# Performance work log

Hardware: AMD Instinct MI355X
Metric: run time of the kernel (lower is better)

## Reference

```python
import jax, jax.numpy as jnp
import numpy as np

D = 64
NEG = 0.01            # leakyrelu_neg_slope
X_CONN = 0.25         # x_connection_init
SKIP_H = 0.5          # skip_weight_h
SIGMAS = np.asarray(1.5 ** np.arange(15), np.float32)  # all_sigmas_dist

N_LIG, N_REC = 4096, 8192
E_LIG, E_REC = 65536, 262144
F_LIG, F_REC, NRBF = 15, 27, 15


def _lrelu(x):
    return jax.nn.leaky_relu(x, NEG)


def _ln(x, g, b, eps=1e-5):
    m = x.mean(-1, keepdims=True)
    v = ((x - m) ** 2).mean(-1, keepdims=True)
    return (x - m) * jax.lax.rsqrt(v + eps) * g + b


def _mlp2(x, w1, b1, g, bt, w2, b2):
    # nn.Sequential(Linear, Dropout(0), LeakyReLU, LayerNorm, Linear) in eval mode
    return _ln(_lrelu(x @ w1 + b1), g, bt) @ w2 + b2


def _coords_mlp(m, w1, b1, w2, b2):
    # nn.Sequential(Linear, Dropout(0), LeakyReLU, Linear(out,1))
    return _lrelu(m @ w1 + b1) @ w2 + b2  # [E, 1]


def _seg_mean(v, idx, n):
    # DGL fn.mean over incoming edges at destination nodes (0 for isolated nodes)
    s = jax.ops.segment_sum(v, idx, num_segments=n)
    c = jax.ops.segment_sum(jnp.ones(idx.shape, v.dtype), idx, num_segments=n)
    return s / jnp.maximum(c, 1.0)[:, None]


def setup_inputs() -> dict:
    key = jax.random.key(0)
    ks = iter(jax.random.split(key, 64))

    def n(shape, s=1.0):
        return jax.random.normal(next(ks), shape, jnp.float32) * s

    def lin(i, o):
        return n((i, o), 1.0 / float(np.sqrt(i)))

    zeros = lambda *s: jnp.zeros(s, jnp.float32)
    ones = lambda *s: jnp.ones(s, jnp.float32)

    d = {}
    d['coords_lig'] = n((N_LIG, 3))
    d['h_lig'] = n((N_LIG, D))
    d['orig_h_lig'] = n((N_LIG, D))
    d['orig_coords_lig'] = n((N_LIG, 3))
    d['coords_rec'] = n((N_REC, 3))
    d['h_rec'] = n((N_REC, D))
    d['orig_h_rec'] = n((N_REC, D))
    d['orig_coords_rec'] = n((N_REC, 3))
    d['lig_src'] = jax.random.randint(next(ks), (E_LIG,), 0, N_LIG)
    d['lig_dst'] = jax.random.randint(next(ks), (E_LIG,), 0, N_LIG)
    d['lig_efeat'] = n((E_LIG, F_LIG))
    d['rec_src'] = jax.random.randint(next(ks), (E_REC,), 0, N_REC)
    d['rec_dst'] = jax.random.randint(next(ks), (E_REC,), 0, N_REC)
    d['rec_efeat'] = n((E_REC, F_REC))
    d['mask'] = (jax.random.uniform(next(ks), (N_LIG, N_REC)) < 0.5).astype(jnp.float32)
    # ---- parameters ----
    d['lig_em_w1'], d['lig_em_b1'] = lin(2 * D + F_LIG + NRBF, D), zeros(D)
    d['lig_em_g'], d['lig_em_bt'] = ones(D), zeros(D)
    d['lig_em_w2'], d['lig_em_b2'] = lin(D, D), zeros(D)
    d['rec_em_w1'], d['rec_em_b1'] = lin(2 * D + F_REC + NRBF, D), zeros(D)
    d['rec_em_g'], d['rec_em_bt'] = ones(D), zeros(D)
    d['rec_em_w2'], d['rec_em_b2'] = lin(D, D), zeros(D)
    d['lig_cm_w1'], d['lig_cm_b1'] = lin(D, D), zeros(D)
    d['lig_cm_w2'], d['lig_cm_b2'] = lin(D, 1), zeros(1)
    d['rec_cm_w1'], d['rec_cm_b1'] = lin(D, D), zeros(D)
    d['rec_cm_w2'], d['rec_cm_b2'] = lin(D, 1), zeros(1)
    for nm in ['q_lig_w', 'k_lig_w', 'v_lig_w', 'q_rec_w', 'k_rec_w', 'v_rec_w']:
        d[nm] = lin(D, D)
    d['lig_nm_w1'], d['lig_nm_b1'] = lin(4 * D, D), zeros(D)
    d['lig_nm_g'], d['lig_nm_bt'] = ones(D), zeros(D)
    d['lig_nm_w2'], d['lig_nm_b2'] = lin(D, D), zeros(D)
    d['rec_nm_w1'], d['rec_nm_b1'] = lin(4 * D, D), zeros(D)
    d['rec_nm_g'], d['rec_nm_bt'] = ones(D), zeros(D)
    d['rec_nm_w2'], d['rec_nm_b2'] = lin(D, D), zeros(D)
    return d


def reference(coords_lig, h_lig, orig_h_lig, orig_coords_lig,
              coords_rec, h_rec, orig_h_rec, orig_coords_rec,
              lig_src, lig_dst, lig_efeat, rec_src, rec_dst, rec_efeat, mask,
              lig_em_w1, lig_em_b1, lig_em_g, lig_em_bt, lig_em_w2, lig_em_b2,
              rec_em_w1, rec_em_b1, rec_em_g, rec_em_bt, rec_em_w2, rec_em_b2,
              lig_cm_w1, lig_cm_b1, lig_cm_w2, lig_cm_b2,
              rec_cm_w1, rec_cm_b1, rec_cm_w2, rec_cm_b2,
              q_lig_w, k_lig_w, v_lig_w, q_rec_w, k_rec_w, v_rec_w,
              lig_nm_w1, lig_nm_b1, lig_nm_g, lig_nm_bt, lig_nm_w2, lig_nm_b2,
              rec_nm_w1, rec_nm_b1, rec_nm_g, rec_nm_bt, rec_nm_w2, rec_nm_b2):
    n_lig, n_rec = coords_lig.shape[0], coords_rec.shape[0]
    sig = jnp.asarray(SIGMAS, coords_lig.dtype)

    # --- ligand edge messages: x_rel = x_src - x_dst, multi-scale RBF of |x_rel|^2 ---
    xr_l = coords_lig[lig_src] - coords_lig[lig_dst]                       # [E_l, 3]
    rbf_l = jnp.exp(-jnp.sum(xr_l * xr_l, -1, keepdims=True) / sig)        # [E_l, 15]
    msg_l = _mlp2(jnp.concatenate([h_lig[lig_src], h_lig[lig_dst], lig_efeat, rbf_l], -1),
                  lig_em_w1, lig_em_b1, lig_em_g, lig_em_bt, lig_em_w2, lig_em_b2)

    # --- receptor edge messages (rec_square_distance_scale = 1) ---
    xr_r = coords_rec[rec_src] - coords_rec[rec_dst]
    rbf_r = jnp.exp(-jnp.sum(xr_r * xr_r, -1, keepdims=True) / sig)
    msg_r = _mlp2(jnp.concatenate([h_rec[rec_src], h_rec[rec_dst], rec_efeat, rbf_r], -1),
                  rec_em_w1, rec_em_b1, rec_em_g, rec_em_bt, rec_em_w2, rec_em_b2)

    # --- masked cross-graph attention (pre/post cross-msg norms are identity) ---
    q_l, k_l, v_l = _lrelu(h_lig @ q_lig_w), _lrelu(h_lig @ k_lig_w), h_lig @ v_lig_w
    q_r, k_r, v_r = _lrelu(h_rec @ q_rec_w), _lrelu(h_rec @ k_rec_w), h_rec @ v_rec_w
    s_lr = mask * (q_l @ k_r.T) - 1000.0 * (1.0 - mask)
    att_l = jax.nn.softmax(s_lr, axis=1) @ v_r                             # [N_l, D]
    mt = mask.T
    s_rl = mt * (q_r @ k_l.T) - 1000.0 * (1.0 - mt)
    att_r = jax.nn.softmax(s_rl, axis=1) @ v_l                             # [N_r, D]

    # --- equivariant coordinate update: mean_j phi_x(m_ij) * x_rel, + skip to orig ---
    coef_l = _coords_mlp(msg_l, lig_cm_w1, lig_cm_b1, lig_cm_w2, lig_cm_b2)
    x_lig = X_CONN * orig_coords_lig + (1.0 - X_CONN) * coords_lig + _seg_mean(xr_l * coef_l, lig_dst, n_lig)
    coef_r = _coords_mlp(msg_r, rec_cm_w1, rec_cm_b1, rec_cm_w2, rec_cm_b2)
    x_rec = X_CONN * orig_coords_rec + (1.0 - X_CONN) * coords_rec + _seg_mean(xr_r * coef_r, rec_dst, n_rec)

    # --- node feature update with skip (h_feats_dim == out_feats_dim) ---
    aggr_l = _seg_mean(msg_l, lig_dst, n_lig)
    h_lig_out = SKIP_H * _mlp2(jnp.concatenate([h_lig, aggr_l, att_l, orig_h_lig], -1),
                               lig_nm_w1, lig_nm_b1, lig_nm_g, lig_nm_bt, lig_nm_w2, lig_nm_b2) \
        + (1.0 - SKIP_H) * h_lig
    aggr_r = _seg_mean(msg_r, rec_dst, n_rec)
    h_rec_out = SKIP_H * _mlp2(jnp.concatenate([h_rec, aggr_r, att_r, orig_h_rec], -1),
                               rec_nm_w1, rec_nm_b1, rec_nm_g, rec_nm_bt, rec_nm_w2, rec_nm_b2) \
        + (1.0 - SKIP_H) * h_rec
    return x_lig, h_lig_out, x_rec, h_rec_out
```

## Files before the change

kernel.cpp:

```cpp
#include <hip/hip_runtime.h>
#include <hip/hip_bf16.h>

typedef __hip_bfloat16 bf16;
typedef __attribute__((ext_vector_type(8))) short bfrag8;
typedef __attribute__((ext_vector_type(4))) float f32x4;

#define N_LIG 4096
#define N_REC 8192
#define E_LIG 65536
#define E_REC 262144
#define F_LIGc 15
#define F_RECc 27

__device__ __forceinline__ float ldkv(const float* p, size_t i) { return p[i]; }
__device__ __forceinline__ float ldkv(const bf16* p, size_t i) { return __bfloat162float(p[i]); }
__device__ __forceinline__ short bfbits(float x) {
    bf16 b = __float2bfloat16(x);
    return *(short*)&b;
}
__device__ __forceinline__ unsigned short stg(const float* p, size_t i) {
    return (unsigned short)bfbits(p[i]);
}
__device__ __forceinline__ unsigned short stg(const bf16* p, size_t i) {
    return *(const unsigned short*)(p + i);
// ... 204 lines not shown
        int e = idx / 15, s5 = idx - e * 15;
        xb[e * KP + 128 + F + s5] = bfbits(__expf(-d2s[e] * c_inv_sigma[s5]));
    }
    {
        constexpr int PER = K1S * 32 - IN;
        for (int idx = t; idx < 64 * PER; idx += 256) {
            int e = idx / PER, k = idx - e * PER;
            xb[e * KP + IN + k] = 0;
        }
    }
    __syncthreads();

    float vreg[4][4];
    #pragma unroll
    for (int m = 0; m < 4; ++m) {
        f32x4 acc = {0.f, 0.f, 0.f, 0.f};
        #pragma unroll
        for (int kk = 0; kk < K1S; ++kk) {
            bfrag8 a = *(const bfrag8*)&xb[(m * 16 + lm) * KP + kk * 32 + qd * 8];
            acc = __builtin_amdgcn_mfma_f32_16x16x32_bf16(a, w1f[kk], acc, 0, 0, 0);
        }
        #pragma unroll
        for (int r = 0; r < 4; ++r) {
            float v = acc[r] + b1n;
            v = v > 0.f ? v : 0.01f * v;
            vreg[m][r] = v;
            float a1 = v, a2 = v * v;
            a1 += __shfl_xor(a1, 1); a2 += __shfl_xor(a2, 1);
            a1 += __shfl_xor(a1, 2); a2 += __shfl_xor(a2, 2);
            a1 += __shfl_xor(a1, 4); a2 += __shfl_xor(a2, 4);
            a1 += __shfl_xor(a1, 8); a2 += __shfl_xor(a2, 8);
            if (lm == 0) {
                wsum1[wv][m * 16 + qd * 4 + r] = a1;
                wsum2[wv][m * 16 + qd * 4 + r] = a2;
            }
        }
    }
    __syncthreads();
    if (t < 64) {
        float s1 = wsum1[0][t] + wsum1[1][t] + wsum1[2][t] + wsum1[3][t];
        float s2 = wsum2[0][t] + wsum2[1][t] + wsum2[2][t] + wsum2[3][t];
        float mean = s1 * (1.f / 64.f);
        float var = s2 * (1.f / 64.f) - mean * mean;
        stat_m[t] = mean;
        stat_r[t] = rsqrtf(fmaxf(var, 0.f) + 1e-5f);
    }
    __syncthreads();

    #pragma unroll
    for (int m = 0; m < 4; ++m)
        #pragma unroll
        for (int r = 0; r < 4; ++r) {
            int row = m * 16 + qd * 4 + r;
            float v = (vreg[m][r] - stat_m[row]) * stat_r[row] * gn + btn;
            h1b[row * 72 + n] = bfbits(v);
        }
    __syncthreads();

    f32x4 acc2[4];
    #pragma unroll
    for (int m = 0; m < 4; ++m) {
        f32x4 acc = {0.f, 0.f, 0.f, 0.f};
        #pragma unroll
        for (int kk = 0; kk < 2; ++kk) {
            bfrag8 a = *(const bfrag8*)&h1b[(m * 16 + lm) * 72 + kk * 32 + qd * 8];
            acc = __builtin_amdgcn_mfma_f32_16x16x32_bf16(a, w2f[kk], acc, 0, 0, 0);
        }
        acc2[m] = acc;
    }
    __syncthreads();
    #pragma unroll
    for (int m = 0; m < 4; ++m)
        #pragma unroll
        for (int r = 0; r < 4; ++r)
            msgf[(m * 16 + qd * 4 + r) * 68 + n] = acc2[m][r] + b2n;
    __syncthreads();

    {
        int j = t & 63, q = t >> 6;
        float acc = 0.f;
        #pragma unroll
        for (int e = q * 16; e < q * 16 + 16; ++e) {
            acc += msgf[e * 68 + j];
            bool flush = (e - q * 16 == 15) || (dsts[e + 1] != dsts[e]);
            if (flush) {
                atomicAdd(&aggr[(size_t)dsts[e] * 64 + j], acc);
                acc = 0.f;
            }
        }
    }

    bfrag8 c1f[2];
    #pragma unroll
    for (int kk = 0; kk < 2; ++kk)
        c1f[kk] = *(const bfrag8*)&c1p[((size_t)(kk * 4 + wv) * 64 + L) * 8];
    #pragma unroll
    for (int m = 0; m < 4; ++m) {
        f32x4 acc = {0.f, 0.f, 0.f, 0.f};
        #pragma unroll
        for (int kk = 0; kk < 2; ++kk) {
            const float* mp = &msgf[(m * 16 + lm) * 68 + kk * 32 + qd * 8];
            f32x4 p0 = *(const f32x4*)mp;
            f32x4 p1 = *(const f32x4*)(mp + 4);
            unsigned short tb[8];
            #pragma unroll
            for (int j = 0; j < 4; ++j) {
                tb[j]     = (unsigned short)bfbits(p0[j]);
                tb[4 + j] = (unsigned short)bfbits(p1[j]);
            }
            bfrag8 a = *(bfrag8*)tb;
            acc = __builtin_amdgcn_mfma_f32_16x16x32_bf16(a, c1f[kk], acc, 0, 0, 0);
        }
        #pragma unroll
        for (int r = 0; r < 4; ++r) {
            float v = acc[r] + cb1n;
            v = v > 0.f ? v : 0.01f * v;
            v *= cw2n;
            v += __shfl_xor(v, 1);
            v += __shfl_xor(v, 2);
            v += __shfl_xor(v, 4);
            v += __shfl_xor(v, 8);
            if (lm == 0) coefp[wv][m * 16 + qd * 4 + r] = v;
        }
    }
    __syncthreads();
    if (t < 64)
        coef_all[t] = coefp[0][t] + coefp[1][t] + coefp[2][t] + coefp[3][t] + cb2[0];
    __syncthreads();

    if (t < 12) {
        int q = t / 3, ax = t - q * 3;
        float acc = 0.f;
        for (int e = q * 16; e < q * 16 + 16; ++e) {
            acc += xr_s[e][ax] * coef_all[e];
            bool flush = (e - q * 16 == 15) || (dsts[e + 1] != dsts[e]);
            if (flush) {
                atomicAdd(&xacc[dsts[e] * 3 + ax], acc);
                acc = 0.f;
            }
        }
    }
}

__global__ __launch_bounds__(256, 3) void node_mfma(
    int nbl,
    const float* h1, const float* __restrict__ aggr1, const int* __restrict__ cnt1,
    const float* att1, const float* __restrict__ origh1,
    const float* __restrict__ w1a, const float* __restrict__ b1a,
    const float* __restrict__ ga, const float* __restrict__ bta,
    const float* __restrict__ w2a, const float* __restrict__ b2a, float* out1,
    const float* h2, const float* __restrict__ aggr2, const int* __restrict__ cnt2,
    const float* att2, const float* __restrict__ origh2,
    const float* __restrict__ w1b, const float* __restrict__ b1b,
    const float* __restrict__ gb, const float* __restrict__ btb,
    const float* __restrict__ w2b, const float* __restrict__ b2b, float* out2)
{
    const float *h, *aggr, *att, *orig_h, *w1, *b1, *g, *bt, *w2, *b2;
    const int* cnt;
    float* h_out;
    int n0;
    if ((int)blockIdx.x < nbl) {
        h = h1; aggr = aggr1; cnt = cnt1; att = att1; orig_h = origh1;
        w1 = w1a; b1 = b1a; g = ga; bt = bta; w2 = w2a; b2 = b2a; h_out = out1;
        n0 = blockIdx.x * 64;
    } else {
        h = h2; aggr = aggr2; cnt = cnt2; att = att2; orig_h = origh2;
        w1 = w1b; b1 = b1b; g = gb; bt = btb; w2 = w2b; b2 = b2b; h_out = out2;
        n0 = (blockIdx.x - nbl) * 64;
    }

    constexpr int KP = 264;
    __shared__ __align__(16) char smem[64 * KP * 2];
    __shared__ __align__(16) unsigned short h1b[64 * 72];
    __shared__ float sums[256], sums2[256];
    __shared__ float stat_m[64], stat_r[64];
    unsigned short* xb  = (unsigned short*)smem;
    float*          h1f = (float*)smem;

    const int t  = threadIdx.x;
    const int lm = t & 15;
    const int qd = (t & 63) >> 4;
    const int n  = (t >> 6) * 16 + lm;

    bfrag8 w1f[8], w2f[2];
    #pragma unroll
    for (int kk = 0; kk < 8; ++kk)
        #pragma unroll
        for (int j = 0; j < 8; ++j) {
            int k = kk * 32 + qd * 8 + j;
            w1f[kk][j] = bfbits(w1[k * 64 + n]);
        }
    #pragma unroll
    for (int kk = 0; kk < 2; ++kk)
        #pragma unroll
        for (int j = 0; j < 8; ++j) {
            int k = kk * 32 + qd * 8 + j;
            w2f[kk][j] = bfbits(w2[k * 64 + n]);
        }
    const float b1n = b1[n], b2n = b2[n];

    for (int p = 0; p < 16; ++p) {
        int e = (t >> 6) + 4 * p;
        int node = n0 + e;
        float invc = 1.f / fmaxf((float)cnt[node], 1.f);
        int j = t & 63;
        xb[e * KP + j]       = bfbits(h[(size_t)node * 64 + j]);
        xb[e * KP + 64 + j]  = bfbits(aggr[(size_t)node * 64 + j] * invc);
        xb[e * KP + 128 + j] = bfbits(att[(size_t)node * 64 + j]);
        xb[e * KP + 192 + j] = bfbits(orig_h[(size_t)node * 64 + j]);
    }
    __syncthreads();

    f32x4 acc1[4];
    #pragma unroll
    for (int m = 0; m < 4; ++m) {
        f32x4 acc = {0.f, 0.f, 0.f, 0.f};
        #pragma unroll
        for (int kk = 0; kk < 8; ++kk) {
            bfrag8 a = *(const bfrag8*)&xb[(m * 16 + lm) * KP + kk * 32 + qd * 8];
            acc = __builtin_amdgcn_mfma_f32_16x16x32_bf16(a, w1f[kk], acc, 0, 0, 0);
        }
        acc1[m] = acc;
    }
    __syncthreads();
    #pragma unroll
    for (int m = 0; m < 4; ++m)
        #pragma unroll
        for (int r = 0; r < 4; ++r) {
            int mr = m * 16 + qd * 4 + r;
            float v = acc1[m][r] + b1n;
            v = v > 0.f ? v : 0.01f * v;
            h1f[mr * 68 + n] = v;
        }
    __syncthreads();

    {
        int e = t >> 2, seg = (t & 3) * 16;
        float s1 = 0.f, s2 = 0.f;
        #pragma unroll
        for (int j = 0; j < 16; ++j) {
            float v = h1f[e * 68 + seg + j];
            s1 += v; s2 += v * v;
        }
        sums[t] = s1; sums2[t] = s2;
    }
    __syncthreads();
    if (t < 64) {
        float s1 = sums[4 * t] + sums[4 * t + 1] + sums[4 * t + 2] + sums[4 * t + 3];
        float s2 = sums2[4 * t] + sums2[4 * t + 1] + sums2[4 * t + 2] + sums2[4 * t + 3];
        float mean = s1 * (1.f / 64.f);
        float var = s2 * (1.f / 64.f) - mean * mean;
        stat_m[t] = mean;
        stat_r[t] = rsqrtf(fmaxf(var, 0.f) + 1e-5f);
    }
    __syncthreads();
    for (int idx = t; idx < 4096; idx += 256) {
        int e = idx >> 6, j = idx & 63;
        float v = (h1f[e * 68 + j] - stat_m[e]) * stat_r[e] * g[j] + bt[j];
        h1b[e * 72 + j] = bfbits(v);
    }
    __syncthreads();

    #pragma unroll
    for (int m = 0; m < 4; ++m) {
        f32x4 acc = {0.f, 0.f, 0.f, 0.f};
        #pragma unroll
        for (int kk = 0; kk < 2; ++kk) {
            bfrag8 a = *(const bfrag8*)&h1b[(m * 16 + lm) * 72 + kk * 32 + qd * 8];
            acc = __builtin_amdgcn_mfma_f32_16x16x32_bf16(a, w2f[kk], acc, 0, 0, 0);
        }
        #pragma unroll
        for (int r = 0; r < 4; ++r) {
            int row = n0 + m * 16 + qd * 4 + r;
            float o = acc[r] + b2n;
            float hv = h[(size_t)row * 64 + n];
            h_out[(size_t)row * 64 + n] = 0.5f * o + 0.5f * hv;
        }
    }
}

__global__ __launch_bounds__(256) void kv_proj_kernel(
    const float* __restrict__ h_lig, const float* __restrict__ h_rec,
    const float* __restrict__ kwl, const float* __restrict__ vwl,
    const float* __restrict__ kwr, const float* __restrict__ vwr,
    bf16* __restrict__ kbl, bf16* __restrict__ vbl,
    bf16* __restrict__ kbr, bf16* __restrict__ vbr)
{
    int job = blockIdx.x * 4 + (threadIdx.x >> 6);
    int j = threadIdx.x & 63;
    const float *h, *w; bf16* out; int node, do_l;
    if (job < N_LIG)                { h = h_lig; w = kwl; out = kbl; node = job;                   do_l = 1; }
    else if (job < 2 * N_LIG)       { h = h_lig; w = vwl; out = vbl; node = job - N_LIG;           do_l = 0; }
    else if (job < 2 * N_LIG + N_REC) { h = h_rec; w = kwr; out = kbr; node = job - 2 * N_LIG;     do_l = 1; }
    else                            { h = h_rec; w = vwr; out = vbr; node = job - 2 * N_LIG - N_REC; do_l = 0; }
    float xv = h[(size_t)node * 64 + j];
    float acc = 0.f;
    #pragma unroll
    for (int i = 0; i < 64; ++i) acc += __shfl(xv, i, 64) * w[i * 64 + j];
    if (do_l) acc = acc > 0.f ? acc : 0.01f * acc;
    out[(size_t)node * 64 + j] = __float2bfloat16(acc);
}

__global__ __launch_bounds__(256) void build_masks(
    const float* __restrict__ mask, unsigned char* __restrict__ m8,
    unsigned char* __restrict__ m8T, int R, int C)
{
    __shared__ __align__(16) unsigned char tl[64 * 80];
    int r0 = blockIdx.y * 64, c0 = blockIdx.x * 64;
    int t = threadIdx.x;
    int cs = (t & 15) * 4;
    #pragma unroll
    for (int rr = 0; rr < 4; ++rr) {
        int r = (t >> 4) + rr * 16;
        unsigned b0 = (mask[(size_t)(r0 + r) * C + c0 + cs + 0] != 0.f);
        unsigned b1 = (mask[(size_t)(r0 + r) * C + c0 + cs + 1] != 0.f);
        unsigned b2 = (mask[(size_t)(r0 + r) * C + c0 + cs + 2] != 0.f);
        unsigned b3 = (mask[(size_t)(r0 + r) * C + c0 + cs + 3] != 0.f);
        *(unsigned*)&m8[(size_t)(r0 + r) * C + c0 + cs] = b0 | (b1 << 8) | (b2 << 16) | (b3 << 24);
        tl[(cs + 0) * 80 + r] = (unsigned char)b0;
        tl[(cs + 1) * 80 + r] = (unsigned char)b1;
        tl[(cs + 2) * 80 + r] = (unsigned char)b2;
        tl[(cs + 3) * 80 + r] = (unsigned char)b3;
    }
    __syncthreads();
    {
        int c = t >> 2, rs = (t & 3) * 16;
        *(uint4*)&m8T[(size_t)(c0 + c) * R + r0 + rs] = *(const uint4*)&tl[c * 80 + rs];
    }
}

template <int MMODE>
__global__ __launch_bounds__(256, 4) void attn_mfma(
    int nb1,
    const float* __restrict__ h1, const float* __restrict__ qw1,
    const bf16* __restrict__ k1, const bf16* __restrict__ v1,
    const unsigned char* __restrict__ m81, const float* __restrict__ mf1, long mrs1, long mcs1,
    float* __restrict__ pO1, float* __restrict__ pM1, float* __restrict__ pL1,
    int nrows1, int ncols1, int nsplit1,
    const float* __restrict__ h2, const float* __restrict__ qw2,
    const bf16* __restrict__ k2, const bf16* __restrict__ v2,
    const unsigned char* __restrict__ m82, const float* __restrict__ mf2, long mrs2, long mcs2,
    float* __restrict__ pO2, float* __restrict__ pM2, float* __restrict__ pL2,
    int nrows2, int ncols2, int nsplit2)
{
    const float *h, *qw, *mf;
    const bf16 *kkp, *vvp;
    const unsigned char* m8;
    long mrs, mcs;
    float *pO, *pM, *pL;
    int n_rows, n_cols, nsplit, bid;
    if ((int)blockIdx.x < nb1) {
        h = h1; qw = qw1; kkp = k1; vvp = v1; m8 = m81; mf = mf1; mrs = mrs1; mcs = mcs1;
        pO = pO1; pM = pM1; pL = pL1; n_rows = nrows1; n_cols = ncols1; nsplit = nsplit1;
        bid = blockIdx.x;
    } else {
        h = h2; qw = qw2; kkp = k2; vvp = v2; m8 = m82; mf = mf2; mrs = mrs2; mcs = mcs2;
        pO = pO2; pM = pM2; pL = pL2; n_rows = nrows2; n_cols = ncols2; nsplit = nsplit2;
        bid = blockIdx.x - nb1;
    }

    const int t  = threadIdx.x;
    const int wv = t >> 6;
    const int lm = t & 15;
    const int qd = (t & 63) >> 4;
    const int rb = bid / nsplit;
    const int sp = bid - rb * nsplit;
    const int r0 = rb * 64;
    const int cols_per = n_cols / nsplit;
    const int c_begin = sp * cols_per;

    __shared__ __align__(16) unsigned short sQ[64 * 64];
    __shared__ __align__(16) unsigned short sP[64 * 64];
    __shared__ __align__(16) unsigned short sK[64 * 64];
    __shared__ __align__(16) unsigned short sV[64 * 64];
    __shared__ __align__(16) unsigned char mt[64 * 80];

    const int cP = t >> 3, segP = (t & 7) * 8;
    const int rM = t >> 2, segM = (t & 3) * 16;

    #pragma unroll
    for (int u = 0; u < 2; ++u) {
        int rr = cP + 32 * u;
        const float* hp = h + (size_t)(r0 + rr) * 64 + segP;
        unsigned short tmp[8];
        #pragma unroll
        for (int j = 0; j < 8; ++j) tmp[j] = bfbits(hp[j]);
        *(uint4*)&sP[swz(rr, segP)] = *(uint4*)tmp;
        const float* qp = qw + (size_t)rr * 64 + segP;
        #pragma unroll
        for (int j = 0; j < 8; ++j) sK[swz(segP + j, rr)] = bfbits(qp[j]);
    }

    uint4 kreg[2], vreg[2], mreg;
    kreg[0] = *(const uint4*)(kkp + (size_t)(c_begin + cP) * 64 + segP);
    kreg[1] = *(const uint4*)(kkp + (size_t)(c_begin + cP + 32) * 64 + segP);
    vreg[0] = *(const uint4*)(vvp + (size_t)(c_begin + cP) * 64 + segP);
    vreg[1] = *(const uint4*)(vvp + (size_t)(c_begin + cP + 32) * 64 + segP);
    if (MMODE == 0)
        mreg = *(const uint4*)&m8[(size_t)(r0 + rM) * n_cols + c_begin + segM];
    __syncthreads();

    {
        bfrag8 a0 = *(const bfrag8*)&sP[swz(wv * 16 + lm, qd * 8)];
        bfrag8 a1 = *(const bfrag8*)&sP[swz(wv * 16 + lm, 32 + qd * 8)];
        #pragma unroll
        for (int ns = 0; ns < 4; ++ns) {
            f32x4 acc = {0.f, 0.f, 0.f, 0.f};
            bfrag8 b0 = *(const bfrag8*)&sK[swz(ns * 16 + lm, qd * 8)];
            bfrag8 b1 = *(const bfrag8*)&sK[swz(ns * 16 + lm, 32 + qd * 8)];
            acc = __builtin_amdgcn_mfma_f32_16x16x32_bf16(a0, b0, acc, 0, 0, 0);
            acc = __builtin_amdgcn_mfma_f32_16x16x32_bf16(a1, b1, acc, 0, 0, 0);
            #pragma unroll
            for (int r = 0; r < 4; ++r) {
                float v = acc[r];
                v = v > 0.f ? v : 0.01f * v;
                sQ[swz(wv * 16 + qd * 4 + r, ns * 16 + lm)] = bfbits(v);
            }
        }
    }
    __syncthreads();

    float rm[4], rl[4];
    #pragma unroll
    for (int r = 0; r < 4; ++r) { rm[r] = -1e30f; rl[r] = 0.f; }
    f32x4 o[4];
    #pragma unroll
    for (int ds = 0; ds < 4; ++ds) o[ds] = (f32x4){0.f, 0.f, 0.f, 0.f};

    const int nt = cols_per / 64;
    for (int tile = 0; tile < nt; ++tile) {
        #pragma unroll
        for (int u = 0; u < 2; ++u) {
            *(uint4*)&sK[swz(cP + 32 * u, segP)] = kreg[u];
            unsigned short* pr = (unsigned short*)&vreg[u];
            #pragma unroll
            for (int j = 0; j < 8; ++j) sV[swz(segP + j, cP + 32 * u)] = pr[j];
        }
        if (MMODE == 0) {
            *(uint4*)&mt[rM * 80 + segM] = mreg;
        } else {
            int c0 = c_begin + tile * 64;
            #pragma unroll
            for (int u = 0; u < 16; ++u) {
                int i = t + 256 * u;
                int r = i >> 6, c = i & 63;
                mt[r * 80 + c] = (unsigned char)(
                    mf[(size_t)(r0 + r) * mrs + (size_t)(c0 + c) * mcs] != 0.f);
            }
        }
        __syncthreads();

        if (tile + 1 < nt) {
            int c0n = c_begin + (tile + 1) * 64;
            kreg[0] = *(const uint4*)(kkp + (size_t)(c0n + cP) * 64 + segP);
            kreg[1] = *(const uint4*)(kkp + (size_t)(c0n + cP + 32) * 64 + segP);
            vreg[0] = *(const uint4*)(vvp + (size_t)(c0n + cP) * 64 + segP);
            vreg[1] = *(const uint4*)(vvp + (size_t)(c0n + cP + 32) * 64 + segP);
            if (MMODE == 0)
                mreg = *(const uint4*)&m8[(size_t)(r0 + rM) * n_cols + c0n + segM];
        }

        f32x4 s[4];
        {
            bfrag8 a0 = *(const bfrag8*)&sQ[swz(wv * 16 + lm, qd * 8)];
            bfrag8 a1 = *(const bfrag8*)&sQ[swz(wv * 16 + lm, 32 + qd * 8)];
            #pragma unroll
            for (int ns = 0; ns < 4; ++ns) {
                f32x4 acc = {0.f, 0.f, 0.f, 0.f};
                bfrag8 b0 = *(const bfrag8*)&sK[swz(ns * 16 + lm, qd * 8)];
                bfrag8 b1 = *(const bfrag8*)&sK[swz(ns * 16 + lm, 32 + qd * 8)];
                acc = __builtin_amdgcn_mfma_f32_16x16x32_bf16(a0, b0, acc, 0, 0, 0);
                acc = __builtin_amdgcn_mfma_f32_16x16x32_bf16(a1, b1, acc, 0, 0, 0);
                s[ns] = acc;
            }
        }

        float alpha[4];
        #pragma unroll
        for (int r = 0; r < 4; ++r) {
            int rloc = wv * 16 + qd * 4 + r;
            float v0 = mt[rloc * 80 +  0 + lm] ? s[0][r] : -1000.f;
            float v1 = mt[rloc * 80 + 16 + lm] ? s[1][r] : -1000.f;
            float v2 = mt[rloc * 80 + 32 + lm] ? s[2][r] : -1000.f;
            float v3 = mt[rloc * 80 + 48 + lm] ? s[3][r] : -1000.f;
            float mx = quad_max(fmaxf(fmaxf(v0, v1), fmaxf(v2, v3)));
            float mn = fmaxf(rm[r], mx);
            float al = __expf(rm[r] - mn);
            rm[r] = mn; alpha[r] = al;
            float p0 = __expf(v0 - mn), p1 = __expf(v1 - mn);
            float p2 = __expf(v2 - mn), p3 = __expf(v3 - mn);
            sP[swz(rloc,  0 + lm)] = bfbits(p0);
            sP[swz(rloc, 16 + lm)] = bfbits(p1);
            sP[swz(rloc, 32 + lm)] = bfbits(p2);
            sP[swz(rloc, 48 + lm)] = bfbits(p3);
            float ls = quad_sum(p0 + p1 + p2 + p3);
            rl[r] = rl[r] * al + ls;
        }
        #pragma unroll
        for (int ds = 0; ds < 4; ++ds)
            #pragma unroll
            for (int r = 0; r < 4; ++r) o[ds][r] *= alpha[r];

        __builtin_amdgcn_wave_barrier();
        asm volatile("" ::: "memory");

        {
            bfrag8 a0 = *(const bfrag8*)&sP[swz(wv * 16 + lm, qd * 8)];
            bfrag8 a1 = *(const bfrag8*)&sP[swz(wv * 16 + lm, 32 + qd * 8)];
            #pragma unroll
            for (int ds = 0; ds < 4; ++ds) {
                bfrag8 b0 = *(const bfrag8*)&sV[swz(ds * 16 + lm, qd * 8)];
                bfrag8 b1 = *(const bfrag8*)&sV[swz(ds * 16 + lm, 32 + qd * 8)];
                o[ds] = __builtin_amdgcn_mfma_f32_16x16x32_bf16(a0, b0, o[ds], 0, 0, 0);
                o[ds] = __builtin_amdgcn_mfma_f32_16x16x32_bf16(a1, b1, o[ds], 0, 0, 0);
            }
        }
        __syncthreads();
    }

    #pragma unroll
    for (int ds = 0; ds < 4; ++ds)
        #pragma unroll
        for (int r = 0; r < 4; ++r) {
            int row = r0 + wv * 16 + qd * 4 + r;
            pO[((size_t)sp * n_rows + row) * 64 + ds * 16 + lm] = o[ds][r];
        }
    if (lm == 0) {
        #pragma unroll
        for (int r = 0; r < 4; ++r) {
            int row = r0 + wv * 16 + qd * 4 + r;
            pM[(size_t)sp * n_rows + row] = rm[r];
            pL[(size_t)sp * n_rows + row] = rl[r];
        }
    }
}

__global__ __launch_bounds__(64) void attn_merge2(
    const float* __restrict__ pO1, const float* __restrict__ pM1, const float* __restrict__ pL1,
    float* __restrict__ out1, int ns1,
    const float* __restrict__ pO2, const float* __restrict__ pM2, const float* __restrict__ pL2,
    float* __restrict__ out2, int ns2)
{
    int r = blockIdx.x;
    const float *pO, *pM, *pL; float* out; int n_rows, nsplit;
    if (r < N_LIG) { pO = pO1; pM = pM1; pL = pL1; out = out1; n_rows = N_LIG; nsplit = ns1; }
    else { r -= N_LIG; pO = pO2; pM = pM2; pL = pL2; out = out2; n_rows = N_REC; nsplit = ns2; }
    int d = threadIdx.x;
    float mstar = -1e30f;
    for (int s = 0; s < nsplit; ++s) mstar = fmaxf(mstar, pM[(size_t)s * n_rows + r]);
    float L = 0.f, O = 0.f;
    for (int s = 0; s < nsplit; ++s) {
        float w = __expf(pM[(size_t)s * n_rows + r] - mstar);
        L += pL[(size_t)s * n_rows + r] * w;
        O += pO[((size_t)s * n_rows + r) * 64 + d] * w;
    }
    out[(size_t)r * 64 + d] = O / L;
}

__global__ __launch_bounds__(256) void attn_row_kernel(
    const float* __restrict__ h, const float* __restrict__ qw,
    const bf16* __restrict__ k, const bf16* __restrict__ v,
    const float* __restrict__ mask, long mrs, long mcs,
    float* __restrict__ out, int n_cols)
{
    int row = blockIdx.x;
    int tid = threadIdx.x;
    extern __shared__ float sc[];
    __shared__ float hrow[64];
    __shared__ float qrow[64];
    __shared__ float red[4];
    __shared__ float opart[4][64];

    if (tid < 64) hrow[tid] = h[(size_t)row * 64 + tid];
    __syncthreads();
    if (tid < 64) {
        float a = 0.f;
        #pragma unroll 8
        for (int i = 0; i < 64; ++i) a += hrow[i] * qw[i * 64 + tid];
        qrow[tid] = a > 0.f ? a : 0.01f * a;
    }
    __syncthreads();

    float lmax = -1e30f;
    for (int c = tid; c < n_cols; c += 256) {
        const bf16* kr = k + (size_t)c * 64;
        float s = 0.f;
        #pragma unroll 8
        for (int i = 0; i < 64; ++i) s += qrow[i] * ldkv(kr, i);
        float m = mask[(size_t)row * mrs + (size_t)c * mcs];
        s = m * s - 1000.f * (1.f - m);
        sc[c] = s;
        lmax = fmaxf(lmax, s);
    }
    #pragma unroll
    for (int o = 32; o > 0; o >>= 1) lmax = fmaxf(lmax, __shfl_xor(lmax, o, 64));
    int wid = tid >> 6;
    if ((tid & 63) == 0) red[wid] = lmax;
    __syncthreads();
    float bmax = fmaxf(fmaxf(red[0], red[1]), fmaxf(red[2], red[3]));
    __syncthreads();

    float lsum = 0.f;
    for (int c = tid; c < n_cols; c += 256) {
        float e = __expf(sc[c] - bmax);
        sc[c] = e;
        lsum += e;
    }
    lsum = wave_sum(lsum);
    if ((tid & 63) == 0) red[wid] = lsum;
    __syncthreads();
    float inv = 1.f / (red[0] + red[1] + red[2] + red[3]);

    int dd = tid & 63;
    float o = 0.f;
    for (int c = wid; c < n_cols; c += 4) o += sc[c] * ldkv(v, (size_t)c * 64 + dd);
    opart[wid][dd] = o;
    __syncthreads();
    if (wid == 0)
        out[(size_t)row * 64 + dd] =
            (opart[0][dd] + opart[1][dd] + opart[2][dd] + opart[3][dd]) * inv;
}

__global__ void coord2_kernel(
    const float* __restrict__ ol, const float* __restrict__ cl,
    const float* __restrict__ xl, const int* __restrict__ cntl, float* __restrict__ outl,
    const float* __restrict__ orr, const float* __restrict__ cr,
    const float* __restrict__ xr, const int* __restrict__ cntr, float* __restrict__ outr)
{
    int i = blockIdx.x * 256 + threadIdx.x;
    if (i < N_LIG * 3) {
        int node = i / 3;
        float invc = 1.f / fmaxf((float)cntl[node], 1.f);
        outl[i] = 0.25f * ol[i] + 0.75f * cl[i] + xl[i] * invc;
        return;
    }
    i -= N_LIG * 3;
    if (i < N_REC * 3) {
        int node = i / 3;
        float invc = 1.f / fmaxf((float)cntr[node], 1.f);
        outr[i] = 0.25f * orr[i] + 0.75f * cr[i] + xr[i] * invc;
    }
}

extern "C" void kernel_launch(void* const* d_in, const int* in_sizes, int n_in,
                              void* d_out, int out_size, void* d_ws, size_t ws_size,
                              hipStream_t stream)
{
    const float* coords_lig      = (const float*)d_in[0];
    const float* h_lig           = (const float*)d_in[1];
    const float* orig_h_lig      = (const float*)d_in[2];
    const float* orig_coords_lig = (const float*)d_in[3];
    const float* coords_rec      = (const float*)d_in[4];
    const float* h_rec           = (const float*)d_in[5];
    const float* orig_h_rec      = (const float*)d_in[6];
    const float* orig_coords_rec = (const float*)d_in[7];
    const int* lig_src   = (const int*)d_in[8];
    const int* lig_dst   = (const int*)d_in[9];
    const float* lig_efeat = (const float*)d_in[10];
    const int* rec_src   = (const int*)d_in[11];
    const int* rec_dst   = (const int*)d_in[12];
    const float* rec_efeat = (const float*)d_in[13];
    const float* mask      = (const float*)d_in[14];
    const float *lig_em_w1 = (const float*)d_in[15], *lig_em_b1 = (const float*)d_in[16];
    const float *lig_em_g  = (const float*)d_in[17], *lig_em_bt = (const float*)d_in[18];
    const float *lig_em_w2 = (const float*)d_in[19], *lig_em_b2 = (const float*)d_in[20];
    const float *rec_em_w1 = (const float*)d_in[21], *rec_em_b1 = (const float*)d_in[22];
    const float *rec_em_g  = (const float*)d_in[23], *rec_em_bt = (const float*)d_in[24];
    const float *rec_em_w2 = (const float*)d_in[25], *rec_em_b2 = (const float*)d_in[26];
    const float *lig_cm_w1 = (const float*)d_in[27], *lig_cm_b1 = (const float*)d_in[28];
    const float *lig_cm_w2 = (const float*)d_in[29], *lig_cm_b2 = (const float*)d_in[30];
    const float *rec_cm_w1 = (const float*)d_in[31], *rec_cm_b1 = (const float*)d_in[32];
    const float *rec_cm_w2 = (const float*)d_in[33], *rec_cm_b2 = (const float*)d_in[34];
    const float *q_lig_w = (const float*)d_in[35], *k_lig_w = (const float*)d_in[36];
    const float *v_lig_w = (const float*)d_in[37], *q_rec_w = (const float*)d_in[38];
    const float *k_rec_w = (const float*)d_in[39], *v_rec_w = (const float*)d_in[40];
    const float *lig_nm_w1 = (const float*)d_in[41], *lig_nm_b1 = (const float*)d_in[42];
    const float *lig_nm_g  = (const float*)d_in[43], *lig_nm_bt = (const float*)d_in[44];
    const float *lig_nm_w2 = (const float*)d_in[45], *lig_nm_b2 = (const float*)d_in[46];
    const float *rec_nm_w1 = (const float*)d_in[47], *rec_nm_b1 = (const float*)d_in[48];
    const float *rec_nm_g  = (const float*)d_in[49], *rec_nm_bt = (const float*)d_in[50];
    const float *rec_nm_w2 = (const float*)d_in[51], *rec_nm_b2 = (const float*)d_in[52];

    char* wsb = (char*)d_ws;
    float* aggr_l = (float*)(wsb + 16);
    float* aggr_r = aggr_l + (size_t)N_LIG * 64;
    float* xacc_l = aggr_r + (size_t)N_REC * 64;
    float* xacc_r = xacc_l + (size_t)N_LIG * 3;
    int* counts_l = (int*)(xacc_r + (size_t)N_REC * 3);
    int* counts_r = counts_l + N_LIG;
    const size_t zero_floats =
        (size_t)N_LIG * 64 + (size_t)N_REC * 64 + N_LIG * 3 + N_REC * 3 + N_LIG + N_REC;
    int* cursor_l = counts_r + N_REC;
    int* cursor_r = cursor_l + N_LIG;
    int* order_l  = cursor_r + N_REC;
    int* order_r  = order_l + E_LIG;
    unsigned short* p_rec1  = (unsigned short*)(order_r + E_REC);
    unsigned short* p_lig1  = p_rec1 + 6 * 2048;
    unsigned short* p_rec2  = p_lig1 + 5 * 2048;
    unsigned short* p_lig2  = p_rec2 + 2 * 2048;
    unsigned short* pc_rec1 = p_lig2 + 2 * 2048;
    unsigned short* pc_lig1 = pc_rec1 + 2 * 2048;
    char* kv_base = (char*)(pc_lig1 + 2 * 2048);
    const size_t core_b = (size_t)(kv_base - wsb);
    const size_t kv_b = (size_t)(N_LIG + N_REC) * 64 * 2 * 2;
    const size_t m8_b = (size_t)N_LIG * N_REC;

    const size_t part_b_hi = ((size_t)8 * N_LIG * 64 + (size_t)4 * N_REC * 64) * 4
                           + ((size_t)8 * N_LIG + (size_t)4 * N_REC) * 2 * 4;
    const size_t part_b_lo = ((size_t)4 * N_LIG * 64 + (size_t)2 * N_REC * 64) * 4
                           + ((size_t)4 * N_LIG + (size_t)2 * N_REC) * 2 * 4;

    int tier, ns1, ns2;
    size_t part_b;
    if (ws_size >= core_b + kv_b + part_b_hi + 2 * m8_b) {
        tier = 0; ns1 = 8; ns2 = 4; part_b = part_b_hi;
    } else if (ws_size >= core_b + kv_b + part_b_lo + 2 * m8_b) {
        tier = 0; ns1 = 4; ns2 = 2; part_b = part_b_lo;
    } else if (ws_size >= core_b + kv_b + part_b_lo) {
        tier = 1; ns1 = 4; ns2 = 2; part_b = part_b_lo;
    } else {
        tier = 2; ns1 = 4; ns2 = 2; part_b = part_b_lo;
    }

    bf16* kb_l = (bf16*)kv_base;
    bf16* vb_l = kb_l + (size_t)N_LIG * 64;
    bf16* kb_r = vb_l + (size_t)N_LIG * 64;
    bf16* vb_r = kb_r + (size_t)N_REC * 64;
    float* pO1 = (float*)(kv_base + kv_b);
    float* pO2 = pO1 + (size_t)ns1 * N_LIG * 64;
    float* pM1 = pO2 + (size_t)ns2 * N_REC * 64;
    float* pL1 = pM1 + (size_t)ns1 * N_LIG;
    float* pM2 = pL1 + (size_t)ns1 * N_LIG;
    float* pL2 = pM2 + (size_t)ns2 * N_REC;
    unsigned char* m8  = (unsigned char*)(kv_base + kv_b + part_b);
    unsigned char* m8T = m8 + m8_b;
    bf16* hb_l  = (bf16*)m8;
    bf16* hb_r  = hb_l + (size_t)N_LIG * 64;
    bf16* efb_l = hb_r + (size_t)N_REC * 64;
    bf16* efb_r = efb_l + (size_t)E_LIG * F_LIGc;

    float* out = (float*)d_out;
    float* x_lig_o = out;
    float* h_lig_o = out + 12288;
    float* x_rec_o = out + 274432;
    float* h_rec_o = out + 299008;

    zero_kernel<<<((int)zero_floats + 255) / 256, 256, 0, stream>>>(aggr_l, (int)zero_floats);

    pack_frags<<<19, 256, 0, stream>>>(
        rec_em_w1, lig_em_w1, rec_em_w2, lig_em_w2, rec_cm_w1, lig_cm_w1,
        p_rec1, p_lig1, p_rec2, p_lig2, pc_rec1, pc_lig1);

    hist2_kernel<<<(E_LIG + E_REC) / 256, 256, 0, stream>>>(lig_dst, rec_dst, counts_l, counts_r);
    scan2_kernel<<<2, 256, 0, stream>>>(counts_l, cursor_l, counts_r, cursor_r);
    scatter2_kernel<<<(E_LIG + E_REC) / 256, 256, 0, stream>>>(
        lig_dst, rec_dst, cursor_l, cursor_r, order_l, order_r);

    kv_proj_kernel<<<(2 * (N_LIG + N_REC)) / 4, 256, 0, stream>>>(
        h_lig, h_rec, k_lig_w, v_lig_w, k_rec_w, v_rec_w,
        kb_l, vb_l, kb_r, vb_r);

    if (tier == 0) {
        cvt4_kernel<<<(N_LIG * 64 + N_REC * 64 + E_LIG * F_LIGc + E_REC * F_RECc + 255) / 256,
                      256, 0, stream>>>(
            h_lig, hb_l, N_LIG * 64, h_rec, hb_r, N_REC * 64,
            lig_efeat, efb_l, E_LIG * F_LIGc, rec_efeat, efb_r, E_REC * F_RECc);
        edge_mfma<F_LIGc, 5, bf16><<<E_LIG / 64, 256, 0, stream>>>(
            order_l, coords_lig, hb_l, lig_src, lig_dst, efb_l,
            p_lig1, lig_em_b1, lig_em_g, lig_em_bt, p_lig2, lig_em_b2,
            pc_lig1, lig_cm_b1, lig_cm_w2, lig_cm_b2,
            aggr_l, xacc_l);
        edge_mfma<F_RECc, 6, bf16><<<E_REC / 64, 256, 0, stream>>>(
            order_r, coords_rec, hb_r, rec_src, rec_dst, efb_r,
            p_rec1, rec_em_b1, rec_em_g, rec_em_bt, p_rec2, rec_em_b2,
            pc_rec1, rec_cm_b1, rec_cm_w2, rec_cm_b2,
            aggr_r, xacc_r);
    } else {
        edge_mfma<F_LIGc, 5, float><<<E_LIG / 64, 256, 0, stream>>>(
            order_l, coords_lig, h_lig, lig_src, lig_dst, lig_efeat,
            p_lig1, lig_em_b1, lig_em_g, lig_em_bt, p_lig2, lig_em_b2,
            pc_lig1, lig_cm_b1, lig_cm_w2, lig_cm_b2,
            aggr_l, xacc_l);
        edge_mfma<F_RECc, 6, float><<<E_REC / 64, 256, 0, stream>>>(
            order_r, coords_rec, h_rec, rec_src, rec_dst, rec_efeat,
            p_rec1, rec_em_b1, rec_em_g, rec_em_bt, p_rec2, rec_em_b2,
            pc_rec1, rec_cm_b1, rec_cm_w2, rec_cm_b2,
            aggr_r, xacc_r);
    }

    const int nb1 = (N_LIG / 64) * ns1;
    const int nb2 = (N_REC / 64) * ns2;
    if (tier <= 1) {
        if (tier == 0) {
            dim3 bg(N_REC / 64, N_LIG / 64);
            build_masks<<<bg, 256, 0, stream>>>(mask, m8, m8T, N_LIG, N_REC);
            attn_mfma<0><<<nb1 + nb2, 256, 0, stream>>>(
                nb1,
                h_lig, q_lig_w, kb_r, vb_r, m8, mask, 0L, 0L,
                pO1, pM1, pL1, N_LIG, N_REC, ns1,
                h_rec, q_rec_w, kb_l, vb_l, m8T, mask, 0L, 0L,
                pO2, pM2, pL2, N_REC, N_LIG, ns2);
        } else {
            attn_mfma<1><<<nb1 + nb2, 256, 0, stream>>>(
                nb1,
                h_lig, q_lig_w, kb_r, vb_r, (const unsigned char*)0, mask, (long)N_REC, 1L,
                pO1, pM1, pL1, N_LIG, N_REC, ns1,
                h_rec, q_rec_w, kb_l, vb_l, (const unsigned char*)0, mask, 1L, (long)N_REC,
                pO2, pM2, pL2, N_REC, N_LIG, ns2);
        }
        attn_merge2<<<N_LIG + N_REC, 64, 0, stream>>>(
            pO1, pM1, pL1, h_lig_o, ns1, pO2, pM2, pL2, h_rec_o, ns2);
    } else {
        attn_row_kernel<<<N_LIG, 256, N_REC * sizeof(float), stream>>>(
            h_lig, q_lig_w, kb_r, vb_r, mask, (long)N_REC, 1L, h_lig_o, N_REC);
        attn_row_kernel<<<N_REC, 256, N_LIG * sizeof(float), stream>>>(
            h_rec, q_rec_w, kb_l, vb_l, mask, 1L, (long)N_REC, h_rec_o, N_LIG);
    }

    node_mfma<<<N_LIG / 64 + N_REC / 64, 256, 0, stream>>>(
        N_LIG / 64,
        h_lig, aggr_l, counts_l, h_lig_o, orig_h_lig,
        lig_nm_w1, lig_nm_b1, lig_nm_g, lig_nm_bt, lig_nm_w2, lig_nm_b2, h_lig_o,
        h_rec, aggr_r, counts_r, h_rec_o, orig_h_rec,
        rec_nm_w1, rec_nm_b1, rec_nm_g, rec_nm_bt, rec_nm_w2, rec_nm_b2, h_rec_o);

    coord2_kernel<<<((N_LIG + N_REC) * 3 + 255) / 256, 256, 0, stream>>>(
        orig_coords_lig, coords_lig, xacc_l, counts_l, x_lig_o,
        orig_coords_rec, coords_rec, xacc_r, counts_r, x_rec_o);
}
```

Before: 651.5 us.

## Pack attention masks into 64-bit bitmasks instead of byte masks

The mask preprocessing kernel now emits one 64-bit bitmask per row per 64-column tile, for both the mask and its transpose, in a tile-major layout, instead of byte-per-entry masks. The attention kernel loads one 8-byte word per row per tile (64 threads) and tests bits rather than reading byte tiles from shared memory. This cuts mask write and read traffic by about 8x and shrinks the workspace needed for the fast path. The V transpose store is also unrolled with explicit shifts. The cost is extra bit-packing arithmetic in the preprocessing kernel and a few bit extractions per score.

```diff
diff --git a/kernel.cpp b/kernel.cpp
--- a/kernel.cpp
+++ b/kernel.cpp
@@ -530,30 +530,39 @@
 }
 
 __global__ __launch_bounds__(256) void build_masks(
-    const float* __restrict__ mask, unsigned char* __restrict__ m8,
-    unsigned char* __restrict__ m8T, int R, int C)
-{
-    __shared__ __align__(16) unsigned char tl[64 * 80];
+    const float* __restrict__ mask, unsigned long long* __restrict__ mq,
+    unsigned long long* __restrict__ mqT, int R, int C)
+{
+    __shared__ __align__(4) unsigned char tr[64 * 68];
+    __shared__ __align__(4) unsigned char tc[64 * 68];
     int r0 = blockIdx.y * 64, c0 = blockIdx.x * 64;
     int t = threadIdx.x;
     int cs = (t & 15) * 4;
     #pragma unroll
     for (int rr = 0; rr < 4; ++rr) {
         int r = (t >> 4) + rr * 16;
-        unsigned b0 = (mask[(size_t)(r0 + r) * C + c0 + cs + 0] != 0.f);
-        unsigned b1 = (mask[(size_t)(r0 + r) * C + c0 + cs + 1] != 0.f);
-        unsigned b2 = (mask[(size_t)(r0 + r) * C + c0 + cs + 2] != 0.f);
-        unsigned b3 = (mask[(size_t)(r0 + r) * C + c0 + cs + 3] != 0.f);
-        *(unsigned*)&m8[(size_t)(r0 + r) * C + c0 + cs] = b0 | (b1 << 8) | (b2 << 16) | (b3 << 24);
-        tl[(cs + 0) * 80 + r] = (unsigned char)b0;
-        tl[(cs + 1) * 80 + r] = (unsigned char)b1;
-        tl[(cs + 2) * 80 + r] = (unsigned char)b2;
-        tl[(cs + 3) * 80 + r] = (unsigned char)b3;
-    }
-    __syncthreads();
-    {
-        int c = t >> 2, rs = (t & 3) * 16;
-        *(uint4*)&m8T[(size_t)(c0 + c) * R + r0 + rs] = *(const uint4*)&tl[c * 80 + rs];
+        const float* mp = &mask[(size_t)(r0 + r) * C + c0 + cs];
+        unsigned char b0 = mp[0] != 0.f, b1 = mp[1] != 0.f;
+        unsigned char b2 = mp[2] != 0.f, b3 = mp[3] != 0.f;
+        tr[r * 68 + cs + 0] = b0; tr[r * 68 + cs + 1] = b1;
+        tr[r * 68 + cs + 2] = b2; tr[r * 68 + cs + 3] = b3;
+        tc[(cs + 0) * 68 + r] = b0; tc[(cs + 1) * 68 + r] = b1;
+        tc[(cs + 2) * 68 + r] = b2; tc[(cs + 3) * 68 + r] = b3;
+    }
+    __syncthreads();
+    if (t < 128) {
+        const unsigned* p = (t < 64) ? (const unsigned*)&tr[t * 68]
+                                     : (const unsigned*)&tc[(t - 64) * 68];
+        unsigned lo = 0, hi = 0;
+        #pragma unroll
+        for (int i = 0; i < 8; ++i)
+            lo |= (((p[i] & 0x01010101u) * 0x01020408u) >> 24 & 0xFu) << (4 * i);
+        #pragma unroll
+        for (int i = 8; i < 16; ++i)
+            hi |= (((p[i] & 0x01010101u) * 0x01020408u) >> 24 & 0xFu) << (4 * (i - 8));
+        unsigned long long w = (unsigned long long)lo | ((unsigned long long)hi << 32);
+        if (t < 64) mq[(size_t)(c0 >> 6) * R + r0 + t] = w;
+        else        mqT[(size_t)(r0 >> 6) * C + c0 + (t - 64)] = w;
     }
 }
 
@@ -562,27 +571,27 @@
     int nb1,
     const float* __restrict__ h1, const float* __restrict__ qw1,
     const bf16* __restrict__ k1, const bf16* __restrict__ v1,
-    const unsigned char* __restrict__ m81, const float* __restrict__ mf1, long mrs1, long mcs1,
+    const unsigned long long* __restrict__ mq1, const float* __restrict__ mf1, long mrs1, long mcs1,
     float* __restrict__ pO1, float* __restrict__ pM1, float* __restrict__ pL1,
     int nrows1, int ncols1, int nsplit1,
     const float* __restrict__ h2, const float* __restrict__ qw2,
     const bf16* __restrict__ k2, const bf16* __restrict__ v2,
-    const unsigned char* __restrict__ m82, const float* __restrict__ mf2, long mrs2, long mcs2,
+    const unsigned long long* __restrict__ mq2, const float* __restrict__ mf2, long mrs2, long mcs2,
     float* __restrict__ pO2, float* __restrict__ pM2, float* __restrict__ pL2,
     int nrows2, int ncols2, int nsplit2)
 {
     const float *h, *qw, *mf;
     const bf16 *kkp, *vvp;
-    const unsigned char* m8;
+    const unsigned long long* mq;
     long mrs, mcs;
     float *pO, *pM, *pL;
     int n_rows, n_cols, nsplit, bid;
     if ((int)blockIdx.x < nb1) {
-        h = h1; qw = qw1; kkp = k1; vvp = v1; m8 = m81; mf = mf1; mrs = mrs1; mcs = mcs1;
+        h = h1; qw = qw1; kkp = k1; vvp = v1; mq = mq1; mf = mf1; mrs = mrs1; mcs = mcs1;
         pO = pO1; pM = pM1; pL = pL1; n_rows = nrows1; n_cols = ncols1; nsplit = nsplit1;
         bid = blockIdx.x;
     } else {
-        h = h2; qw = qw2; kkp = k2; vvp = v2; m8 = m82; mf = mf2; mrs = mrs2; mcs = mcs2;
+        h = h2; qw = qw2; kkp = k2; vvp = v2; mq = mq2; mf = mf2; mrs = mrs2; mcs = mcs2;
         pO = pO2; pM = pM2; pL = pL2; n_rows = nrows2; n_cols = ncols2; nsplit = nsplit2;
         bid = blockIdx.x - nb1;
     }
@@ -601,10 +610,10 @@
     __shared__ __align__(16) unsigned short sP[64 * 64];
     __shared__ __align__(16) unsigned short sK[64 * 64];
     __shared__ __align__(16) unsigned short sV[64 * 64];
-    __shared__ __align__(16) unsigned char mt[64 * 80];
+    __shared__ uint2 mtq[64];
+    __shared__ unsigned char mt[64 * 80];
 
     const int cP = t >> 3, segP = (t & 7) * 8;
-    const int rM = t >> 2, segM = (t & 3) * 16;
 
     #pragma unroll
     for (int u = 0; u < 2; ++u) {
@@ -619,13 +628,14 @@
         for (int j = 0; j < 8; ++j) sK[swz(segP + j, rr)] = bfbits(qp[j]);
     }
 
-    uint4 kreg[2], vreg[2], mreg;
+    uint4 kreg[2], vreg[2];
+    unsigned long long mregq = 0;
     kreg[0] = *(const uint4*)(kkp + (size_t)(c_begin + cP) * 64 + segP);
     kreg[1] = *(const uint4*)(kkp + (size_t)(c_begin + cP + 32) * 64 + segP);
     vreg[0] = *(const uint4*)(vvp + (size_t)(c_begin + cP) * 64 + segP);
     vreg[1] = *(const uint4*)(vvp + (size_t)(c_begin + cP + 32) * 64 + segP);
-    if (MMODE == 0)
-        mreg = *(const uint4*)&m8[(size_t)(r0 + rM) * n_cols + c_begin + segM];
+    if (MMODE == 0 && t < 64)
+        mregq = mq[(size_t)(c_begin >> 6) * n_rows + r0 + t];
     __syncthreads();
 
     {
@@ -659,13 +669,20 @@
     for (int tile = 0; tile < nt; ++tile) {
         #pragma unroll
         for (int u = 0; u < 2; ++u) {
-            *(uint4*)&sK[swz(cP + 32 * u, segP)] = kreg[u];
-            unsigned short* pr = (unsigned short*)&vreg[u];
-            #pragma unroll
-            for (int j = 0; j < 8; ++j) sV[swz(segP + j, cP + 32 * u)] = pr[j];
+            int cc = cP + 32 * u;
+            *(uint4*)&sK[swz(cc, segP)] = kreg[u];
+            unsigned x0 = vreg[u].x, x1 = vreg[u].y, x2 = vreg[u].z, x3 = vreg[u].w;
+            sV[swz(segP + 0, cc)] = (unsigned short)x0;
+            sV[swz(segP + 1, cc)] = (unsigned short)(x0 >> 16);
+            sV[swz(segP + 2, cc)] = (unsigned short)x1;
+            sV[swz(segP + 3, cc)] = (unsigned short)(x1 >> 16);
+            sV[swz(segP + 4, cc)] = (unsigned short)x2;
+            sV[swz(segP + 5, cc)] = (unsigned short)(x2 >> 16);
+            sV[swz(segP + 6, cc)] = (unsigned short)x3;
+            sV[swz(segP + 7, cc)] = (unsigned short)(x3 >> 16);
         }
         if (MMODE == 0) {
-            *(uint4*)&mt[rM * 80 + segM] = mreg;
+            if (t < 64) mtq[t] = make_uint2((unsigned)mregq, (unsigned)(mregq >> 32));
         } else {
             int c0 = c_begin + tile * 64;
             #pragma unroll
@@ -684,8 +701,8 @@
             kreg[1] = *(const uint4*)(kkp + (size_t)(c0n + cP + 32) * 64 + segP);
             vreg[0] = *(const uint4*)(vvp + (size_t)(c0n + cP) * 64 + segP);
             vreg[1] = *(const uint4*)(vvp + (size_t)(c0n + cP + 32) * 64 + segP);
-            if (MMODE == 0)
-                mreg = *(const uint4*)&m8[(size_t)(r0 + rM) * n_cols + c0n + segM];
+            if (MMODE == 0 && t < 64)
+                mregq = mq[(size_t)(c0n >> 6) * n_rows + r0 + t];
         }
 
         f32x4 s[4];
@@ -707,10 +724,19 @@
         #pragma unroll
         for (int r = 0; r < 4; ++r) {
             int rloc = wv * 16 + qd * 4 + r;
-            float v0 = mt[rloc * 80 +  0 + lm] ? s[0][r] : -1000.f;
-            float v1 = mt[rloc * 80 + 16 + lm] ? s[1][r] : -1000.f;
-            float v2 = mt[rloc * 80 + 32 + lm] ? s[2][r] : -1000.f;
-            float v3 = mt[rloc * 80 + 48 + lm] ? s[3][r] : -1000.f;
+            float v0, v1, v2, v3;
+            if (MMODE == 0) {
+                uint2 w = mtq[rloc];
+                v0 = (w.x >> lm) & 1        ? s[0][r] : -1000.f;
+                v1 = (w.x >> (16 + lm)) & 1 ? s[1][r] : -1000.f;
+                v2 = (w.y >> lm) & 1        ? s[2][r] : -1000.f;
+                v3 = (w.y >> (16 + lm)) & 1 ? s[3][r] : -1000.f;
+            } else {
+                v0 = mt[rloc * 80 +  0 + lm] ? s[0][r] : -1000.f;
+                v1 = mt[rloc * 80 + 16 + lm] ? s[1][r] : -1000.f;
+                v2 = mt[rloc * 80 + 32 + lm] ? s[2][r] : -1000.f;
+                v3 = mt[rloc * 80 + 48 + lm] ? s[3][r] : -1000.f;
+            }
             float mx = quad_max(fmaxf(fmaxf(v0, v1), fmaxf(v2, v3)));
             float mn = fmaxf(rm[r], mx);
             float al = __expf(rm[r] - mn);
@@ -931,7 +957,13 @@
     char* kv_base = (char*)(pc_lig1 + 2 * 2048);
     const size_t core_b = (size_t)(kv_base - wsb);
     const size_t kv_b = (size_t)(N_LIG + N_REC) * 64 * 2 * 2;
-    const size_t m8_b = (size_t)N_LIG * N_REC;
+
+    const size_t mq1_n = (size_t)(N_REC / 64) * N_LIG;
+    const size_t mq2_n = (size_t)(N_LIG / 64) * N_REC;
+    const size_t mq_all_b = (mq1_n + mq2_n) * 8;
+    const size_t mir_b = (size_t)(N_LIG + N_REC) * 64 * 2
+                       + ((size_t)E_LIG * F_LIGc + (size_t)E_REC * F_RECc) * 2;
+    const size_t region_b = mir_b > mq_all_b ? mir_b : mq_all_b;
 
     const size_t part_b_hi = ((size_t)8 * N_LIG * 64 + (size_t)4 * N_REC * 64) * 4
                            + ((size_t)8 * N_LIG + (size_t)4 * N_REC) * 2 * 4;
@@ -940,9 +972,9 @@
 
     int tier, ns1, ns2;
     size_t part_b;
-    if (ws_size >= core_b + kv_b + part_b_hi + 2 * m8_b) {
+    if (ws_size >= core_b + kv_b + part_b_hi + region_b) {
         tier = 0; ns1 = 8; ns2 = 4; part_b = part_b_hi;
-    } else if (ws_size >= core_b + kv_b + part_b_lo + 2 * m8_b) {
+    } else if (ws_size >= core_b + kv_b + part_b_lo + region_b) {
         tier = 0; ns1 = 4; ns2 = 2; part_b = part_b_lo;
     } else if (ws_size >= core_b + kv_b + part_b_lo) {
         tier = 1; ns1 = 4; ns2 = 2; part_b = part_b_lo;
@@ -960,9 +992,9 @@
     float* pL1 = pM1 + (size_t)ns1 * N_LIG;
     float* pM2 = pL1 + (size_t)ns1 * N_LIG;
     float* pL2 = pM2 + (size_t)ns2 * N_REC;
-    unsigned char* m8  = (unsigned char*)(kv_base + kv_b + part_b);
-    unsigned char* m8T = m8 + m8_b;
-    bf16* hb_l  = (bf16*)m8;
+    unsigned long long* mqb  = (unsigned long long*)(kv_base + kv_b + part_b);
+    unsigned long long* mqbT = mqb + mq1_n;
+    bf16* hb_l  = (bf16*)mqb;
     bf16* hb_r  = hb_l + (size_t)N_LIG * 64;
     bf16* efb_l = hb_r + (size_t)N_REC * 64;
     bf16* efb_r = efb_l + (size_t)E_LIG * F_LIGc;
@@ -1021,19 +1053,19 @@
     if (tier <= 1) {
         if (tier == 0) {
             dim3 bg(N_REC / 64, N_LIG / 64);
-            build_masks<<<bg, 256, 0, stream>>>(mask, m8, m8T, N_LIG, N_REC);
+            build_masks<<<bg, 256, 0, stream>>>(mask, mqb, mqbT, N_LIG, N_REC);
             attn_mfma<0><<<nb1 + nb2, 256, 0, stream>>>(
                 nb1,
-                h_lig, q_lig_w, kb_r, vb_r, m8, mask, 0L, 0L,
+                h_lig, q_lig_w, kb_r, vb_r, mqb, mask, 0L, 0L,
                 pO1, pM1, pL1, N_LIG, N_REC, ns1,
-                h_rec, q_rec_w, kb_l, vb_l, m8T, mask, 0L, 0L,
+                h_rec, q_rec_w, kb_l, vb_l, mqbT, mask, 0L, 0L,
                 pO2, pM2, pL2, N_REC, N_LIG, ns2);
         } else {
             attn_mfma<1><<<nb1 + nb2, 256, 0, stream>>>(
                 nb1,
-                h_lig, q_lig_w, kb_r, vb_r, (const unsigned char*)0, mask, (long)N_REC, 1L,
+                h_lig, q_lig_w, kb_r, vb_r, (const unsigned long long*)0, mask, (long)N_REC, 1L,
                 pO1, pM1, pL1, N_LIG, N_REC, ns1,
-                h_rec, q_rec_w, kb_l, vb_l, (const unsigned char*)0, mask, 1L, (long)N_REC,
+                h_rec, q_rec_w, kb_l, vb_l, (const unsigned long long*)0, mask, 1L, (long)N_REC,
                 pO2, pM2, pL2, N_REC, N_LIG, ns2);
         }
         attn_merge2<<<N_LIG + N_REC, 64, 0, stream>>>(
```

Result: faster. 608.4 us (-6.6%).
